# Optimization experiments

Measured on AMD Instinct MI355X. Metric: run time of the kernel, lower is better.

## Reference

```python
import jax, jax.numpy as jnp
import numpy as np

B, N, DIM = 4, 4096, 768
H = 12
DH = DIM // H          # 64
S = 16                 # num_segments
M = N // S             # 256 segment_len
SCALE = DH ** -0.5


def setup_inputs() -> dict:
    key = jax.random.key(0)
    ks = jax.random.split(key, 7)
    std = DIM ** -0.5
    return {
        "x": jax.random.normal(ks[0], (B, N, DIM), dtype=jnp.float32),
        "Wq": jax.random.normal(ks[1], (DIM, DIM), dtype=jnp.float32) * std,
        "Wkv": jax.random.normal(ks[2], (DIM, DIM), dtype=jnp.float32) * std,
        "Wo": jax.random.normal(ks[3], (DIM, DIM), dtype=jnp.float32) * std,
        "bo": jax.random.normal(ks[4], (DIM,), dtype=jnp.float32) * 0.02,
        "Wo0": jax.random.normal(ks[5], (DIM, DIM), dtype=jnp.float32) * std,
        "bo0": jax.random.normal(ks[6], (DIM,), dtype=jnp.float32) * 0.02,
    }


def _rotary_freqs(n, dh, dtype):
    # lucidrains RotaryEmbedding: inv_freq over even dims, emb = cat(freqs, freqs)
    inv_freq = 1.0 / (10000.0 ** (jnp.arange(0, dh, 2, dtype=jnp.float32) / dh))
    t = jnp.arange(n, dtype=jnp.float32)
    freqs = jnp.einsum("n,f->nf", t, inv_freq)           # (n, dh/2)
    return jnp.concatenate([freqs, freqs], axis=-1).astype(dtype)  # (n, dh)


def _rotate_half(t):
    # '... (j d) -> ... j d', j=2 ; (-x2, x1)
    x1, x2 = jnp.split(t, 2, axis=-1)
    return jnp.concatenate([-x2, x1], axis=-1)


def _apply_rotary(freqs, t):
    # freqs: (1, n, dh) broadcast over (bh, n, dh); rot_dim == dh here
    return t * jnp.cos(freqs) + _rotate_half(t) * jnp.sin(freqs)


def reference(x, Wq, Wkv, Wo, bo, Wo0, bo0):
    b, n, dim = x.shape
    q = x @ Wq            # (b, n, dim), bias-free
    kv = x @ Wkv          # shared K==V projection

    def to_heads(t):      # 'b n (h d) -> (b h) n d'
        return t.reshape(b, n, H, DH).transpose(0, 2, 1, 3).reshape(b * H, n, DH)

    q, kv = to_heads(q), to_heads(kv)

    freqs = _rotary_freqs(n, DH, x.dtype)[None, :, :]    # (1, n, dh)
    q = _apply_rotary(freqs, q)
    kv = _apply_rotary(freqs, kv)

    q = q * SCALE
    c = b * H
    qs = q.reshape(c, S, M, DH)
    kvs = kv.reshape(c, S, M, DH)

    # adjacent-segment KV windows: segment t attends to [t-1, t] for t>=1
    kvs_ccs = jnp.concatenate([kvs[:, :-1], kvs[:, 1:]], axis=2)  # (c, S-1, 2M, dh)
    qs_ccs = qs[:, 1:]                                            # (c, S-1, M, dh)

    lsim = jnp.einsum("csmd,csnd->csmn", qs_ccs, kvs_ccs)         # (c, S-1, M, 2M)
    attn1 = jax.nn.softmax(lsim, axis=-1)
    out1 = jnp.einsum("csmn,csnd->csmd", attn1, kvs_ccs)          # (c, S-1, M, dh)

    # global (self) attention within first segment
    q0, kv0 = qs[:, 0], kvs[:, 0]                                 # (c, M, dh)
    sim0 = jnp.einsum("cmd,cnd->cmn", q0, kv0)
    attn0 = jax.nn.softmax(sim0, axis=-1)
    out0 = jnp.einsum("cmn,cnd->cmd", attn0, kv0)                 # (c, M, dh)

    def merge_heads(t, nn):  # '(b h) nn d -> b nn (h d)'
        return t.reshape(b, H, nn, DH).transpose(0, 2, 1, 3).reshape(b, nn, H * DH)

    out_1 = merge_heads(out1.reshape(c, (S - 1) * M, DH), (S - 1) * M)
    out_0 = merge_heads(out0, M)

    out_1o = out_1 @ Wo + bo
    out_0o = out_0 @ Wo0 + bo0
    return jnp.concatenate([out_0o, out_1o], axis=1)              # (b, n, dim)
```

## Files before the change

kernel.cpp:

```cpp
#include <hip/hip_runtime.h>
#include <hip/hip_bf16.h>


typedef float f32x4 __attribute__((ext_vector_type(4)));
typedef short bf16x8 __attribute__((ext_vector_type(8)));

#define DEV static __device__ __forceinline__

DEV short f2bf(float f) {
  union { __hip_bfloat16 h; unsigned short u; } cv;
  cv.h = __float2bfloat16(f);
  return (short)cv.u;
}

DEV f32x4 fz4() { f32x4 z = {0.f, 0.f, 0.f, 0.f}; return z; }

DEV void gload16(const void* g, void* l) {
  __builtin_amdgcn_global_load_lds((const __attribute__((address_space(1))) void*)g,
                                   (__attribute__((address_space(3))) void*)l, 16, 0, 0);
}

__global__ void __launch_bounds__(256) k_prep(
    const float* __restrict__ x, const float* __restrict__ Wq,
    const float* __restrict__ Wkv, const float* __restrict__ Wo,
    const float* __restrict__ Wo0, short* __restrict__ xb,
    short* __restrict__ WtQKV, short* __restrict__ WtO,
    float2* __restrict__ csT) {
  __shared__ float t[64][65];
  int bid = blockIdx.x;
  if (bid < 512) {
    int idx = bid * 256 + threadIdx.x;
    int pos = idx >> 5, jm = idx & 31;
    float invf = exp2f(-(float)jm * (13.287712379549449f / 32.0f));
    float th = (float)pos * invf;
    csT[idx] = make_float2(cosf(th), sinf(th));
  } else if (bid < 6656) {
    int i = ((bid - 512) * 256 + threadIdx.x) * 8;
    float4 a = *(const float4*)(x + i);
    float4 b = *(const float4*)(x + i + 4);
    bf16x8 v;
    v[0] = f2bf(a.x); v[1] = f2bf(a.y); v[2] = f2bf(a.z); v[3] = f2bf(a.w);
    v[4] = f2bf(b.x); v[5] = f2bf(b.y); v[6] = f2bf(b.z); v[7] = f2bf(b.w);
    *(bf16x8*)(xb + i) = v;
  } else {
    int w = bid - 6656;
    int z = w / 144, rem = w % 144;
    int k0 = (rem / 12) * 64, j0 = (rem % 12) * 64;
    const float* src = (z == 0) ? Wq : (z == 1) ? Wkv : (z == 2) ? Wo : Wo0;
    short* dst = (z < 2) ? (WtQKV + (size_t)z * (768 * 768))
                         : (WtO + (size_t)(z - 2) * (768 * 768));
    int tc = threadIdx.x & 63, tr = threadIdx.x >> 6;
#pragma unroll
    for (int i = 0; i < 16; i++) {
      int r = i * 4 + tr;
      t[tc][r] = src[(size_t)(k0 + r) * 768 + j0 + tc];
    }
    __syncthreads();
#pragma unroll
    for (int i = 0; i < 16; i++) {
      int r = i * 4 + tr;
      dst[(size_t)(j0 + r) * 768 + k0 + tc] = f2bf(t[r][tc]);
    }
  }
}

#define QSTAGE64(Abuf, Bbuf, Abase, Bbase, kt)                                 \
  {                                                                            \
    int cci = (((tid & 7) ^ ((tid >> 3) & 7)) << 4);                           \
    _Pragma("unroll") for (int i = 0; i < 4; i++) {                            \
      int rowi = i * 32 + (tid >> 3);                                          \
      gload16((Abase) + (size_t)(r0 + rowi) * 1536 + (kt) * 128 + cci,         \
              (char*)(Abuf) + i * 4096 + wid * 1024);                          \
      gload16((Bbase) + (size_t)(j0 + rowi) * 1536 + (kt) * 128 + cci,         \
              (char*)(Bbuf) + i * 4096 + wid * 1024);                          \
    }                                                                          \
  }

__global__ void __launch_bounds__(256, 2) k_gemm_qkv(
    const short* __restrict__ xb, const short* __restrict__ Wt,
    const float2* __restrict__ csT,
    short* __restrict__ Qb, short* __restrict__ KVb,
    short* __restrict__ KVtw) {
  __shared__ short Lsh[4][8192];
  int bid = blockIdx.x;
  int xcd = bid & 7, loc = bid >> 3;
  int r0 = (xcd * 16 + loc / 12) * 128;
  int cbk = loc % 12;
  bool isQ = cbk < 6;
  int cbl = isQ ? cbk : cbk - 6;
  const char* Ab = (const char*)xb;
  const char* Bb = (const char*)(Wt + (isQ ? (size_t)0 : (size_t)(768 * 768)));
  int j0 = cbl * 128;
  int tid = threadIdx.x, lane = tid & 63, wid = tid >> 6;
  int wr = wid >> 1, wc = wid & 1;
  int l15 = lane & 15, lg = lane >> 4;
  int swz = (l15 & 7) << 4;

  f32x4 acc[4][4];
#pragma unroll
  for (int i = 0; i < 4; i++)
#pragma unroll
    for (int j = 0; j < 4; j++) acc[i][j] = fz4();

  QSTAGE64(Lsh[0], Lsh[2], Ab, Bb, 0)
  for (int kt = 0; kt < 12; kt++) {
    int cb = kt & 1;
    __syncthreads();
    if (kt + 1 < 12) QSTAGE64(Lsh[cb ^ 1], Lsh[2 + (cb ^ 1)], Ab, Bb, kt + 1)
    const char* Ac = (const char*)Lsh[cb];
    const char* Bc = (const char*)Lsh[2 + cb];
#pragma unroll
    for (int kk = 0; kk < 2; kk++) {
      bf16x8 af[4], bfr[4];
#pragma unroll
      for (int mr = 0; mr < 4; mr++)
        af[mr] = *(const bf16x8*)(Ac + (wr * 64 + mr * 16 + l15) * 128 +
                                  ((kk * 64 + lg * 16) ^ swz));
#pragma unroll
      for (int nc = 0; nc < 4; nc++)
        bfr[nc] = *(const bf16x8*)(Bc + (wc * 64 + nc * 16 + l15) * 128 +
                                   ((kk * 64 + lg * 16) ^ swz));
#pragma unroll
      for (int mr = 0; mr < 4; mr++)
#pragma unroll
        for (int nc = 0; nc < 4; nc++)
          acc[mr][nc] = __builtin_amdgcn_mfma_f32_16x16x32_bf16(af[mr], bfr[nc], acc[mr][nc], 0, 0, 0);
    }
  }

  int h = 2 * cbl + wc;
  short* Ob = isQ ? Qb : KVb;
  float scl = isQ ? 0.18033688011112042f : 1.0f;
  short ovv[4][4][4];
#pragma unroll
  for (int mr = 0; mr < 4; mr++) {
#pragma unroll
    for (int rg = 0; rg < 4; rg++) {
      int r = r0 + wr * 64 + mr * 16 + lg * 4 + rg;
      int b = r >> 12, pos = r & 4095;
      const float2* cp = csT + pos * 32;
      float2 cs0 = cp[l15], cs1 = cp[16 + l15];
      float v0 = acc[mr][0][rg], v1 = acc[mr][1][rg];
      float v2 = acc[mr][2][rg], v3 = acc[mr][3][rg];
      short o0 = f2bf((v0 * cs0.x - v2 * cs0.y) * scl);
      short o1 = f2bf((v1 * cs1.x - v3 * cs1.y) * scl);
      short o2 = f2bf((v2 * cs0.x + v0 * cs0.y) * scl);
      short o3 = f2bf((v3 * cs1.x + v1 * cs1.y) * scl);
      size_t base = ((size_t)((b * 12 + h) * 4096 + pos)) * 64 + l15;
      Ob[base] = o0; Ob[base + 16] = o1; Ob[base + 32] = o2; Ob[base + 48] = o3;
      ovv[mr][rg][0] = o0; ovv[mr][rg][1] = o1;
      ovv[mr][rg][2] = o2; ovv[mr][rg][3] = o3;
    }
  }

  if (!isQ && KVtw) {
    __syncthreads();
    short* Ovt = (short*)Lsh;
#pragma unroll
    for (int mr = 0; mr < 4; mr++)
#pragma unroll
      for (int rg = 0; rg < 4; rg++) {
        int p = wr * 64 + mr * 16 + lg * 4 + rg;
        int w = p & 31, g = p >> 5;
        int sig = 8 * ((w & 15) >> 2) + 4 * ((w >> 4) & 1) + (w & 3);
        int pi = g * 32 + sig;
#pragma unroll
        for (int nc = 0; nc < 4; nc++) {
          int row = wc * 64 + nc * 16 + l15;
          Ovt[row * 136 + (pi ^ ((row & 3) << 4))] = ovv[mr][rg][nc];
        }
      }
    __syncthreads();
    int b = r0 >> 12, pos0 = r0 & 4095;
#pragma unroll
    for (int z = 0; z < 8; z++) {
      int rr = z * 16 + (tid >> 4);
      int chunk = tid & 15;
      int off = rr * 136 + ((chunk * 8) ^ ((rr & 3) << 4));
      bf16x8 v = *(const bf16x8*)&Ovt[off];
      int wcr = rr >> 6, d = rr & 63;
      *(bf16x8*)&KVtw[((size_t)((b * 12 + 2 * cbl + wcr) * 64 + d)) * 4096 +
                      pos0 + chunk * 8] = v;
    }
  }
}

__global__ void __launch_bounds__(256) k_transkv(const short* __restrict__ KVb,
                                                 short* __restrict__ KVt) {
  __shared__ short T[64][72];
  int c = blockIdx.x;
  int pt = blockIdx.y;
  int t = threadIdx.x;
  int ch = t & 7, rr = t >> 3;
#pragma unroll
  for (int i = 0; i < 2; i++) {
    int p = rr + i * 32;
    bf16x8 v = *(const bf16x8*)&KVb[((size_t)c * 4096 + pt * 64 + p) * 64 + ch * 8];
    *(bf16x8*)&T[p][ch * 8] = v;
  }
  __syncthreads();
#pragma unroll
  for (int i = 0; i < 2; i++) {
    int d = rr + i * 32;
    bf16x8 v;
#pragma unroll
    for (int j = 0; j < 8; j++) {
      int cc = ch * 8 + j;
      int g = cc >> 5, sig = cc & 31;
      int p = g * 32 + 4 * (sig >> 3) + (sig & 3) + 16 * ((sig >> 2) & 1);
      v[j] = T[p][d];
    }
    *(bf16x8*)&KVt[((size_t)c * 64 + d) * 4096 + pt * 64 + ch * 8] = v;
  }
}

#define STAGE(buf, kk0)                                                        \
  {                                                                            \
    _Pragma("unroll") for (int i = 0; i < 2; i++) {                            \
      gload16(KVc + (size_t)((kk0) + i * 32 + krow) * 128 + ksrccol,           \
              (char*)Kl[buf] + i * 4096 + wid * 1024);                         \
      gload16(KVtc + ((size_t)(i * 32 + krow) * 4096 + (kk0)) * 2 + ksrccol,   \
              (char*)Vl[buf] + i * 4096 + wid * 1024);                         \
    }                                                                          \
  }

__global__ void __launch_bounds__(256, 4) k_attn(const short* __restrict__ Qb,
                                                 const short* __restrict__ KVbp,
                                                 const short* __restrict__ KVtp,
                                                 short* __restrict__ AO) {
  __shared__ short Kl[2][4096];
  __shared__ short Vl[2][4096];
  int bid = blockIdx.x;
  int orig = (bid & 7) * 192 + (bid >> 3);
  int c = orig >> 5;
  int e = orig & 31;
  int s = (e < 2) ? 0 : ((e - 2) >> 1) + 1;
  int qh = (e < 2) ? e : (e - 2) & 1;
  int NC = (s == 0) ? 4 : 8;
  int Kbase = (s == 0) ? 0 : (s - 1) * 256;

  int tid = threadIdx.x, lane = tid & 63, wid = tid >> 6;
  int l15 = lane & 15, lg = lane >> 4;
  const char* KVc = (const char*)(KVbp + (size_t)c * 4096 * 64);
  const char* KVtc = (const char*)(KVtp + (size_t)c * 64 * 4096);

  int krow = tid >> 3;
  int ksrccol = ((tid & 7) * 16) ^ ((krow & 7) << 4);
  int swz = (l15 & 7) << 4;

  int q0 = s * 256 + qh * 128 + wid * 32;
  bf16x8 qf[2][2];
#pragma unroll
  for (int qt = 0; qt < 2; qt++) {
    const short* Qr = Qb + ((size_t)c * 4096 + q0 + qt * 16 + l15) * 64 + lg * 8;
    qf[qt][0] = *(const bf16x8*)Qr;
    qf[qt][1] = *(const bf16x8*)(Qr + 32);
  }

  const f32x4 mi = {-32.f, -32.f, -32.f, -32.f};
  bf16x8 ones;
#pragma unroll
  for (int j = 0; j < 8; j++) ones[j] = (short)0x3F80;

  f32x4 oacc[2][4];
  f32x4 lacc[2];
#pragma unroll
  for (int qt = 0; qt < 2; qt++) {
    lacc[qt] = fz4();
#pragma unroll
    for (int vt = 0; vt < 4; vt++) oacc[qt][vt] = fz4();
  }

  STAGE(0, Kbase)
  for (int ch = 0; ch < NC; ch++) {
    int cb = ch & 1;
    __syncthreads();
    if (ch + 1 < NC) STAGE(cb ^ 1, Kbase + (ch + 1) * 64)
    const char* Kb_ = (const char*)Kl[cb];
    const char* Vb_ = (const char*)Vl[cb];
#pragma unroll
    for (int u = 0; u < 2; u++) {
      f32x4 z[2][2];
#pragma unroll
      for (int t2 = 0; t2 < 2; t2++) {
        const char* Kp = Kb_ + ((2 * u + t2) * 16 + l15) * 128;
        bf16x8 kf0 = *(const bf16x8*)(Kp + ((lg * 16) ^ swz));
        bf16x8 kf1 = *(const bf16x8*)(Kp + ((64 + lg * 16) ^ swz));
        __builtin_amdgcn_s_setprio(1);
#pragma unroll
        for (int qt = 0; qt < 2; qt++) {
          f32x4 zz = __builtin_amdgcn_mfma_f32_16x16x32_bf16(kf0, qf[qt][0], mi, 0, 0, 0);
          zz = __builtin_amdgcn_mfma_f32_16x16x32_bf16(kf1, qf[qt][1], zz, 0, 0, 0);
          z[qt][t2] = zz;
        }
        __builtin_amdgcn_s_setprio(0);
      }
      bf16x8 pf[2];
#pragma unroll
      for (int qt = 0; qt < 2; qt++) {
#pragma unroll
        for (int t2 = 0; t2 < 2; t2++)
#pragma unroll
          for (int r = 0; r < 4; r++)
            pf[qt][t2 * 4 + r] = f2bf(exp2f(z[qt][t2][r]));
      }
      bf16x8 vf[4];
#pragma unroll
      for (int vt = 0; vt < 4; vt++)
        vf[vt] = *(const bf16x8*)(Vb_ + (vt * 16 + l15) * 128 +
                                  ((u * 64 + lg * 16) ^ swz));
      __builtin_amdgcn_s_setprio(1);
#pragma unroll
      for (int qt = 0; qt < 2; qt++) {
#pragma unroll
        for (int vt = 0; vt < 4; vt++)
          oacc[qt][vt] = __builtin_amdgcn_mfma_f32_16x16x32_bf16(pf[qt], vf[vt], oacc[qt][vt], 0, 0, 0);
        lacc[qt] = __builtin_amdgcn_mfma_f32_16x16x32_bf16(pf[qt], ones, lacc[qt], 0, 0, 0);
      }
      __builtin_amdgcn_s_setprio(0);
    }
  }

  int bq = c / 12, hh = c % 12;
#pragma unroll
  for (int qt = 0; qt < 2; qt++) {
    float rinv[4];
#pragma unroll
    for (int r = 0; r < 4; r++) rinv[r] = 1.0f / lacc[qt][r];
#pragma unroll
    for (int vt = 0; vt < 4; vt++)
#pragma unroll
      for (int r = 0; r < 4; r++) {
        size_t row = (size_t)bq * 4096 + q0 + qt * 16 + lg * 4 + r;
        AO[row * 768 + hh * 64 + vt * 16 + l15] = f2bf(oacc[qt][vt][r] * rinv[r]);
      }
  }
}

__global__ void __launch_bounds__(256, 2) k_gemm_out(
    const short* __restrict__ AO, const short* __restrict__ Wt,
    const float* __restrict__ bo, const float* __restrict__ bo0,
    float* __restrict__ out) {
  __shared__ short Lsh[4][8192];
  int bid = blockIdx.x;
  int xcd = bid & 7, loc = bid >> 3;
  int r0 = (xcd * 16 + loc / 6) * 128;
  int j0 = (loc % 6) * 128;
  bool o0sel = (r0 & 4095) < 256;
  const char* Ab = (const char*)AO;
  const char* Bb = (const char*)(Wt + (o0sel ? (size_t)1 : (size_t)0) * (768 * 768));
  const float* bias = o0sel ? bo0 : bo;
  int tid = threadIdx.x, lane = tid & 63, wid = tid >> 6;
  int wr = wid >> 1, wc = wid & 1;
  int l15 = lane & 15, lg = lane >> 4;
  int swz = (l15 & 7) << 4;

  f32x4 acc[4][4];
#pragma unroll
  for (int i = 0; i < 4; i++)
#pragma unroll
    for (int j = 0; j < 4; j++) acc[i][j] = fz4();

  QSTAGE64(Lsh[0], Lsh[2], Ab, Bb, 0)
  for (int kt = 0; kt < 12; kt++) {
    int cb = kt & 1;
    __syncthreads();
    if (kt + 1 < 12) QSTAGE64(Lsh[cb ^ 1], Lsh[2 + (cb ^ 1)], Ab, Bb, kt + 1)
    const char* Ac = (const char*)Lsh[cb];
    const char* Bc = (const char*)Lsh[2 + cb];
#pragma unroll
    for (int kk = 0; kk < 2; kk++) {
      bf16x8 af[4], bfr[4];
#pragma unroll
      for (int mr = 0; mr < 4; mr++)
        af[mr] = *(const bf16x8*)(Ac + (wr * 64 + mr * 16 + l15) * 128 +
                                  ((kk * 64 + lg * 16) ^ swz));
#pragma unroll
      for (int nc = 0; nc < 4; nc++)
        bfr[nc] = *(const bf16x8*)(Bc + (wc * 64 + nc * 16 + l15) * 128 +
                                   ((kk * 64 + lg * 16) ^ swz));
#pragma unroll
      for (int mr = 0; mr < 4; mr++)
#pragma unroll
        for (int nc = 0; nc < 4; nc++)
          acc[mr][nc] = __builtin_amdgcn_mfma_f32_16x16x32_bf16(af[mr], bfr[nc], acc[mr][nc], 0, 0, 0);
    }
  }

  float bs[4];
#pragma unroll
  for (int nc = 0; nc < 4; nc++) bs[nc] = bias[j0 + wc * 64 + nc * 16 + l15];
#pragma unroll
  for (int mr = 0; mr < 4; mr++)
#pragma unroll
    for (int rg = 0; rg < 4; rg++) {
      size_t r = (size_t)r0 + wr * 64 + mr * 16 + lg * 4 + rg;
      float* op = out + r * 768 + j0 + wc * 64 + l15;
      op[0]  = acc[mr][0][rg] + bs[0];
      op[16] = acc[mr][1][rg] + bs[1];
      op[32] = acc[mr][2][rg] + bs[2];
      op[48] = acc[mr][3][rg] + bs[3];
    }
}

extern "C" void kernel_launch(void* const* d_in, const int* in_sizes, int n_in,
                              void* d_out, int out_size, void* d_ws, size_t ws_size,
                              hipStream_t stream) {
  (void)in_sizes; (void)n_in; (void)out_size;
  const float* x   = (const float*)d_in[0];
  const float* Wq  = (const float*)d_in[1];
  const float* Wkv = (const float*)d_in[2];
  const float* Wo  = (const float*)d_in[3];
  const float* bo  = (const float*)d_in[4];
  const float* Wo0 = (const float*)d_in[5];
  const float* bo0 = (const float*)d_in[6];
  float* out = (float*)d_out;

  char* ws = (char*)d_ws;
  short* xb  = (short*)(ws + 0);
  short* AO  = xb;
  short* Qb  = (short*)(ws + 25165824);
  short* KVb = (short*)(ws + 50331648);
  short* KVt = (short*)(ws + 75497472);

  bool fused = ws_size >= 106430464u;
  float2* csT;
  short *WtQKV, *WtO;
  if (fused) {
    csT   = (float2*)(ws + 100663296);
    WtQKV = (short*)(ws + 101711872);
    WtO   = (short*)(ws + 104071168);
  } else {
    WtQKV = (short*)(ws + 75497472);
    csT   = (float2*)(ws + 77856768);
    WtO   = (short*)(ws + 100663296);
  }

  k_prep<<<7232, 256, 0, stream>>>(x, Wq, Wkv, Wo, Wo0, xb, WtQKV, WtO, csT);
  k_gemm_qkv<<<1536, 256, 0, stream>>>(xb, WtQKV, csT, Qb, KVb,
                                       fused ? KVt : (short*)nullptr);
  if (!fused) k_transkv<<<dim3(48, 64), 256, 0, stream>>>(KVb, KVt);
  k_attn<<<1536, 256, 0, stream>>>(Qb, KVb, KVt, AO);
  k_gemm_out<<<768, 256, 0, stream>>>(AO, WtO, bo, bo0, out);
}
```

Baseline: 142.6 us.

## Restructure QKV GEMM into 256x128 tiles with 512 threads and fine-grained pipelined staging

The QKV projection GEMM now uses 256-row tiles with 8 waves, 96KB dynamic LDS and separate double-buffered A/B regions. Global-to-LDS loads are interleaved with per-row-block MFMA phases, using explicit vmcnt waits, s_barrier and setprio to overlap memory with compute. The KV transpose staging layout is also reswizzled for the wider tile. This aims to raise operand reuse and hide load latency, at the cost of higher LDS use and fragile hand-scheduled waits, which may limit occupancy.

```diff
diff --git a/kernel.cpp b/kernel.cpp
--- a/kernel.cpp
+++ b/kernel.cpp
@@ -64,33 +64,71 @@
   }
 }
 
-#define QSTAGE64(Abuf, Bbuf, Abase, Bbase, kt)                                 \
+#define GST_A(dstb, T, ii)                                                     \
   {                                                                            \
-    int cci = (((tid & 7) ^ ((tid >> 3) & 7)) << 4);                           \
-    _Pragma("unroll") for (int i = 0; i < 4; i++) {                            \
-      int rowi = i * 32 + (tid >> 3);                                          \
-      gload16((Abase) + (size_t)(r0 + rowi) * 1536 + (kt) * 128 + cci,         \
-              (char*)(Abuf) + i * 4096 + wid * 1024);                          \
-      gload16((Bbase) + (size_t)(j0 + rowi) * 1536 + (kt) * 128 + cci,         \
-              (char*)(Bbuf) + i * 4096 + wid * 1024);                          \
+    int row_ = (ii) * 64 + (tid >> 3);                                         \
+    gload16(Abase + (size_t)(r0 + row_) * 1536 + (size_t)(T) * 128 +           \
+                ((((tid & 7) ^ (row_ & 7)) << 4)),                             \
+            (dstb) + (ii) * 8192 + wid * 1024);                                \
+  }
+#define GST_B(dstb, T, ii)                                                     \
+  {                                                                            \
+    int row_ = (ii) * 64 + (tid >> 3);                                         \
+    gload16(Bbase + (size_t)(j0 + row_) * 1536 + (size_t)(T) * 128 +           \
+                ((((tid & 7) ^ (row_ & 7)) << 4)),                             \
+            (dstb) + (ii) * 8192 + wid * 1024);                                \
+  }
+
+#define VMC2 { asm volatile("s_waitcnt vmcnt(2)" ::: "memory"); __builtin_amdgcn_sched_barrier(0); }
+#define VMC0 { asm volatile("s_waitcnt vmcnt(0)" ::: "memory"); __builtin_amdgcn_sched_barrier(0); }
+
+#define DS_A8(mr, kk) (*(const bf16x8*)(Acur + (wr * 64 + (mr) * 16 + l15) * 128 + \
+                                        (((kk) * 64 + lg * 16) ^ swz)))
+#define DS_B8(nc, kk) (*(const bf16x8*)(Bcur + (wc * 64 + (nc) * 16 + l15) * 128 + \
+                                        (((kk) * 64 + lg * 16) ^ swz)))
+
+#define PH8(mr, VMW)                                                           \
+  {                                                                            \
+    if ((mr) == 0) {                                                           \
+      _Pragma("unroll") for (int n_ = 0; n_ < 4; n_++) {                       \
+        breg[n_][0] = DS_B8(n_, 0);                                            \
+        breg[n_][1] = DS_B8(n_, 1);                                            \
+      }                                                                        \
     }                                                                          \
-  }
-
-__global__ void __launch_bounds__(256, 2) k_gemm_qkv(
+    bf16x8 a0 = DS_A8(mr, 0), a1 = DS_A8(mr, 1);                               \
+    VMW                                                                        \
+    __builtin_amdgcn_s_barrier();                                              \
+    asm volatile("s_waitcnt lgkmcnt(0)" ::: "memory");                         \
+    __builtin_amdgcn_sched_barrier(0);                                         \
+    __builtin_amdgcn_s_setprio(1);                                             \
+    _Pragma("unroll") for (int n_ = 0; n_ < 4; n_++) {                         \
+      acc[mr][n_] = __builtin_amdgcn_mfma_f32_16x16x32_bf16(a0, breg[n_][0], acc[mr][n_], 0, 0, 0); \
+      acc[mr][n_] = __builtin_amdgcn_mfma_f32_16x16x32_bf16(a1, breg[n_][1], acc[mr][n_], 0, 0, 0); \
+    }                                                                          \
+    __builtin_amdgcn_s_setprio(0);                                             \
+    __builtin_amdgcn_s_barrier();                                              \
+  }
+
+__global__ void __launch_bounds__(512, 2) k_gemm_qkv(
     const short* __restrict__ xb, const short* __restrict__ Wt,
     const float2* __restrict__ csT,
     short* __restrict__ Qb, short* __restrict__ KVb,
     short* __restrict__ KVtw) {
-  __shared__ short Lsh[4][8192];
+  extern __shared__ char GL[];
+  char* AL0 = GL;
+  char* AL1 = GL + 32768;
+  char* BL0 = GL + 65536;
+  char* BL1 = GL + 81920;
   int bid = blockIdx.x;
   int xcd = bid & 7, loc = bid >> 3;
-  int r0 = (xcd * 16 + loc / 12) * 128;
-  int cbk = loc % 12;
-  bool isQ = cbk < 6;
-  int cbl = isQ ? cbk : cbk - 6;
-  const char* Ab = (const char*)xb;
-  const char* Bb = (const char*)(Wt + (isQ ? (size_t)0 : (size_t)(768 * 768)));
-  int j0 = cbl * 128;
+  int mb = xcd * 8 + loc / 12;
+  int cbn = loc % 12;
+  bool isQ = cbn < 6;
+  int hb2 = isQ ? cbn : cbn - 6;
+  int r0 = mb * 256;
+  int j0 = hb2 * 128;
+  const char* Abase = (const char*)xb;
+  const char* Bbase = (const char*)(Wt + (isQ ? (size_t)0 : (size_t)(768 * 768)));
   int tid = threadIdx.x, lane = tid & 63, wid = tid >> 6;
   int wr = wid >> 1, wc = wid & 1;
   int l15 = lane & 15, lg = lane >> 4;
@@ -102,41 +140,52 @@
 #pragma unroll
     for (int j = 0; j < 4; j++) acc[i][j] = fz4();
 
-  QSTAGE64(Lsh[0], Lsh[2], Ab, Bb, 0)
-  for (int kt = 0; kt < 12; kt++) {
-    int cb = kt & 1;
-    __syncthreads();
-    if (kt + 1 < 12) QSTAGE64(Lsh[cb ^ 1], Lsh[2 + (cb ^ 1)], Ab, Bb, kt + 1)
-    const char* Ac = (const char*)Lsh[cb];
-    const char* Bc = (const char*)Lsh[2 + cb];
-#pragma unroll
-    for (int kk = 0; kk < 2; kk++) {
-      bf16x8 af[4], bfr[4];
-#pragma unroll
-      for (int mr = 0; mr < 4; mr++)
-        af[mr] = *(const bf16x8*)(Ac + (wr * 64 + mr * 16 + l15) * 128 +
-                                  ((kk * 64 + lg * 16) ^ swz));
-#pragma unroll
-      for (int nc = 0; nc < 4; nc++)
-        bfr[nc] = *(const bf16x8*)(Bc + (wc * 64 + nc * 16 + l15) * 128 +
-                                   ((kk * 64 + lg * 16) ^ swz));
-#pragma unroll
-      for (int mr = 0; mr < 4; mr++)
-#pragma unroll
-        for (int nc = 0; nc < 4; nc++)
-          acc[mr][nc] = __builtin_amdgcn_mfma_f32_16x16x32_bf16(af[mr], bfr[nc], acc[mr][nc], 0, 0, 0);
-    }
-  }
-
-  int h = 2 * cbl + wc;
+  GST_A(AL0, 0, 0) GST_A(AL0, 0, 1) GST_A(AL0, 0, 2) GST_A(AL0, 0, 3)
+  GST_B(BL0, 0, 0) GST_B(BL0, 0, 1)
+  GST_B(BL1, 1, 0) GST_B(BL1, 1, 1)
+  VMC2
+  __builtin_amdgcn_s_barrier();
+
+  for (int t = 0; t < 6; t++) {
+    bool last = (t == 5);
+    {
+      const char* Acur = AL0; const char* Bcur = BL0;
+      bf16x8 breg[4][2];
+      GST_A(AL1, 2 * t + 1, 0) GST_A(AL1, 2 * t + 1, 1)
+      PH8(0, )
+      GST_A(AL1, 2 * t + 1, 2) GST_A(AL1, 2 * t + 1, 3)
+      PH8(1, )
+      if (!last) { GST_B(BL0, 2 * t + 2, 0) }
+      PH8(2, )
+      if (!last) { GST_B(BL0, 2 * t + 2, 1) }
+      PH8(3, if (last) { VMC0 } else { VMC2 })
+    }
+    {
+      const char* Acur = AL1; const char* Bcur = BL1;
+      bf16x8 breg[4][2];
+      if (!last) { GST_A(AL0, 2 * t + 2, 0) GST_A(AL0, 2 * t + 2, 1) }
+      PH8(0, )
+      if (!last) { GST_A(AL0, 2 * t + 2, 2) GST_A(AL0, 2 * t + 2, 3) }
+      PH8(1, )
+      if (!last) { GST_B(BL1, 2 * t + 3, 0) }
+      PH8(2, )
+      if (!last) { GST_B(BL1, 2 * t + 3, 1) }
+      PH8(3, if (!last) { VMC2 })
+    }
+  }
+
+  int h = 2 * hb2 + wc;
   short* Ob = isQ ? Qb : KVb;
   float scl = isQ ? 0.18033688011112042f : 1.0f;
-  short ovv[4][4][4];
+  bool dofuse = (!isQ) && (KVtw != nullptr);
+  short* LB = (short*)GL;
+  if (dofuse) __syncthreads();
 #pragma unroll
   for (int mr = 0; mr < 4; mr++) {
 #pragma unroll
     for (int rg = 0; rg < 4; rg++) {
-      int r = r0 + wr * 64 + mr * 16 + lg * 4 + rg;
+      int p = wr * 64 + mr * 16 + lg * 4 + rg;
+      int r = r0 + p;
       int b = r >> 12, pos = r & 4095;
       const float2* cp = csT + pos * 32;
       float2 cs0 = cp[l15], cs1 = cp[16 + l15];
@@ -148,39 +197,29 @@
       short o3 = f2bf((v3 * cs1.x + v1 * cs1.y) * scl);
       size_t base = ((size_t)((b * 12 + h) * 4096 + pos)) * 64 + l15;
       Ob[base] = o0; Ob[base + 16] = o1; Ob[base + 32] = o2; Ob[base + 48] = o3;
-      ovv[mr][rg][0] = o0; ovv[mr][rg][1] = o1;
-      ovv[mr][rg][2] = o2; ovv[mr][rg][3] = o3;
-    }
-  }
-
-  if (!isQ && KVtw) {
-    __syncthreads();
-    short* Ovt = (short*)Lsh;
-#pragma unroll
-    for (int mr = 0; mr < 4; mr++)
-#pragma unroll
-      for (int rg = 0; rg < 4; rg++) {
-        int p = wr * 64 + mr * 16 + lg * 4 + rg;
+      if (dofuse) {
         int w = p & 31, g = p >> 5;
         int sig = 8 * ((w & 15) >> 2) + 4 * ((w >> 4) & 1) + (w & 3);
         int pi = g * 32 + sig;
+        short ov[4] = {o0, o1, o2, o3};
 #pragma unroll
         for (int nc = 0; nc < 4; nc++) {
-          int row = wc * 64 + nc * 16 + l15;
-          Ovt[row * 136 + (pi ^ ((row & 3) << 4))] = ovv[mr][rg][nc];
+          int rowd = wc * 64 + nc * 16 + l15;
+          LB[rowd * 256 + ((((pi >> 3) ^ (rowd & 31)) << 3) | (pi & 7))] = ov[nc];
         }
       }
+    }
+  }
+  if (dofuse) {
     __syncthreads();
     int b = r0 >> 12, pos0 = r0 & 4095;
 #pragma unroll
     for (int z = 0; z < 8; z++) {
-      int rr = z * 16 + (tid >> 4);
-      int chunk = tid & 15;
-      int off = rr * 136 + ((chunk * 8) ^ ((rr & 3) << 4));
-      bf16x8 v = *(const bf16x8*)&Ovt[off];
-      int wcr = rr >> 6, d = rr & 63;
-      *(bf16x8*)&KVtw[((size_t)((b * 12 + 2 * cbl + wcr) * 64 + d)) * 4096 +
-                      pos0 + chunk * 8] = v;
+      int rr = z * 16 + (tid >> 5);
+      int ck = tid & 31;
+      bf16x8 v = *(const bf16x8*)&LB[rr * 256 + ((ck ^ (rr & 31)) << 3)];
+      *(bf16x8*)&KVtw[((size_t)((b * 12 + 2 * hb2 + (rr >> 6)) * 64 + (rr & 63))) * 4096 +
+                      pos0 + ck * 8] = v;
     }
   }
 }
@@ -336,6 +375,18 @@
       }
   }
 }
+
+#define QSTAGE64(Abuf, Bbuf, Abase2, Bbase2, kt)                               \
+  {                                                                            \
+    int cci = (((tid & 7) ^ ((tid >> 3) & 7)) << 4);                           \
+    _Pragma("unroll") for (int i = 0; i < 4; i++) {                            \
+      int rowi = i * 32 + (tid >> 3);                                          \
+      gload16((Abase2) + (size_t)(r0 + rowi) * 1536 + (kt) * 128 + cci,        \
+              (char*)(Abuf) + i * 4096 + wid * 1024);                          \
+      gload16((Bbase2) + (size_t)(j0 + rowi) * 1536 + (kt) * 128 + cci,        \
+              (char*)(Bbuf) + i * 4096 + wid * 1024);                          \
+    }                                                                          \
+  }
 
 __global__ void __launch_bounds__(256, 2) k_gemm_out(
     const short* __restrict__ AO, const short* __restrict__ Wt,
@@ -437,8 +488,8 @@
   }
 
   k_prep<<<7232, 256, 0, stream>>>(x, Wq, Wkv, Wo, Wo0, xb, WtQKV, WtO, csT);
-  k_gemm_qkv<<<1536, 256, 0, stream>>>(xb, WtQKV, csT, Qb, KVb,
-                                       fused ? KVt : (short*)nullptr);
+  k_gemm_qkv<<<768, 512, 98304, stream>>>(xb, WtQKV, csT, Qb, KVb,
+                                          fused ? KVt : (short*)nullptr);
   if (!fused) k_transkv<<<dim3(48, 64), 256, 0, stream>>>(KVb, KVt);
   k_attn<<<1536, 256, 0, stream>>>(Qb, KVb, KVt, AO);
   k_gemm_out<<<768, 256, 0, stream>>>(AO, WtO, bo, bo0, out);
```

After: 142.6 us. Within noise of the previous version (-0.0%).
